# Performance work log

Measured on AMD Instinct MI355X. Metric: run time of the kernel, lower is better.

The kernel has to match this reference:

```python
import jax, jax.numpy as jnp
import numpy as np
from jax import lax

BN_EPS = 1e-5
NORM_EPS = 1e-8


def _conv(x, w, b, stride, pad):
    y = lax.conv_general_dilated(x, w, (stride, stride), [(pad, pad), (pad, pad)],
                                 dimension_numbers=('NCHW', 'OIHW', 'NCHW'))
    return y + b[None, :, None, None]


def _bn(x, g, b, m, v):
    inv = g / jnp.sqrt(v + BN_EPS)
    return x * inv[None, :, None, None] + (b - m * inv)[None, :, None, None]


def _maxpool2(x):
    return lax.reduce_window(x, -jnp.inf, lax.max, (1, 1, 2, 2), (1, 1, 2, 2), 'VALID')


def setup_inputs() -> dict:
    key = jax.random.key(0)
    ks = jax.random.split(key, 16)
    d = {}
    d['x'] = jax.random.normal(ks[0], (64, 3, 512, 512), dtype=jnp.float32)
    d['conv1_w'] = jax.random.normal(ks[1], (32, 1, 5, 5), jnp.float32) * 0.1
    d['conv1_b'] = jnp.zeros((32,), jnp.float32)
    d['bn1_g'] = jnp.ones((32,), jnp.float32)
    d['bn1_b'] = jnp.zeros((32,), jnp.float32)
    d['bn1_m'] = jax.random.normal(ks[2], (32,), jnp.float32) * 0.1
    d['bn1_v'] = jax.random.uniform(ks[3], (32,), jnp.float32) + 0.5
    d['conv2_w'] = jax.random.normal(ks[4], (64, 32, 3, 3), jnp.float32) * 0.05
    d['conv2_b'] = jnp.zeros((64,), jnp.float32)
    d['bn2_g'] = jnp.ones((64,), jnp.float32)
    d['bn2_b'] = jnp.zeros((64,), jnp.float32)
    d['bn2_m'] = jax.random.normal(ks[5], (64,), jnp.float32) * 0.1
    d['bn2_v'] = jax.random.uniform(ks[6], (64,), jnp.float32) + 0.5
    d['conv3_w'] = jax.random.normal(ks[7], (128, 64, 3, 3), jnp.float32) * 0.04
    d['conv3_b'] = jnp.zeros((128,), jnp.float32)
    d['bn3_g'] = jnp.ones((128,), jnp.float32)
    d['bn3_b'] = jnp.zeros((128,), jnp.float32)
    d['bn3_m'] = jax.random.normal(ks[8], (128,), jnp.float32) * 0.1
    d['bn3_v'] = jax.random.uniform(ks[9], (128,), jnp.float32) + 0.5
    d['fc1_w'] = jax.random.normal(ks[10], (256, 128), jnp.float32) * 0.08
    d['fc1_b'] = jnp.zeros((256,), jnp.float32)
    d['fc2_w'] = jax.random.normal(ks[11], (128, 256), jnp.float32) * 0.06
    d['fc2_b'] = jnp.zeros((128,), jnp.float32)
    return d


def reference(x, conv1_w, conv1_b, bn1_g, bn1_b, bn1_m, bn1_v,
              conv2_w, conv2_b, bn2_g, bn2_b, bn2_m, bn2_v,
              conv3_w, conv3_b, bn3_g, bn3_b, bn3_m, bn3_v,
              fc1_w, fc1_b, fc2_w, fc2_b):
    # ---- batched FFT feature extraction (replaces per-sample numpy loop) ----
    gray = 0.299 * x[:, 0] + 0.587 * x[:, 1] + 0.114 * x[:, 2]      # (B,H,W)
    mag = jnp.abs(jnp.fft.fftshift(jnp.fft.fft2(gray), axes=(-2, -1)))
    logm = jnp.log1p(mag)
    mu = logm.mean(axis=(-2, -1), keepdims=True)
    sd = logm.std(axis=(-2, -1), keepdims=True)
    f = ((logm - mu) / (sd + NORM_EPS))[:, None]                     # (B,1,H,W)
    # ---- conv stack (BatchNorm in inference mode) ----
    h = jax.nn.relu(_bn(_conv(f, conv1_w, conv1_b, 2, 2), bn1_g, bn1_b, bn1_m, bn1_v))
    h = _maxpool2(h)
    h = jax.nn.relu(_bn(_conv(h, conv2_w, conv2_b, 2, 1), bn2_g, bn2_b, bn2_m, bn2_v))
    h = _maxpool2(h)
    h = jax.nn.relu(_bn(_conv(h, conv3_w, conv3_b, 2, 1), bn3_g, bn3_b, bn3_m, bn3_v))
    h = h.mean(axis=(-2, -1))                                        # AdaptiveAvgPool2d(1) -> (B,128)
    # ---- MLP (Dropout is identity in eval) ----
    h = jax.nn.relu(h @ fc1_w.T + fc1_b)
    return jax.nn.relu(h @ fc2_w.T + fc2_b)
```

## Files before the change

kernel.cpp:

```cpp
#include <hip/hip_runtime.h>
#include <math.h>

#define PI_F 3.14159265358979323846f
#define KS 258

typedef float f2 __attribute__((ext_vector_type(2)));

__device__ __forceinline__ void fft512(float* re, float* im,
                                       const float* twr, const float* twi, int u) {
#pragma unroll
  for (int s = 0; s < 8; s += 2) {
    __syncthreads();
    {
      int h  = 1 << s;
      int j  = u & (h - 1);
      int a  = ((u >> s) << (s + 2)) + j;
      int i0 = a, i1 = a + h, i2 = a + 2 * h, i3 = a + 3 * h;
      float e0r = re[i0], e0i = im[i0];
      float e1r = re[i1], e1i = im[i1];
      float e2r = re[i2], e2i = im[i2];
      float e3r = re[i3], e3i = im[i3];
      int tis = j << (8 - s);
      float wsr = twr[tis], wsi = twi[tis];
      float t1r = e1r * wsr - e1i * wsi, t1i = e1r * wsi + e1i * wsr;
      float t3r = e3r * wsr - e3i * wsi, t3i = e3r * wsi + e3i * wsr;
      float b0r = e0r + t1r, b0i = e0i + t1i;
      float b1r = e0r - t1r, b1i = e0i - t1i;
      float b2r = e2r + t3r, b2i = e2i + t3i;
      float b3r = e2r - t3r, b3i = e2i - t3i;
      int ti0 = j << (7 - s);
      int ti1 = (j + h) << (7 - s);
      float w0r = twr[ti0], w0i = twi[ti0];
      float w1r = twr[ti1], w1i = twi[ti1];
      float u2r = b2r * w0r - b2i * w0i, u2i = b2r * w0i + b2i * w0r;
      float u3r = b3r * w1r - b3i * w1i, u3i = b3r * w1i + b3i * w1r;
      re[i0] = b0r + u2r; im[i0] = b0i + u2i;
      re[i2] = b0r - u2r; im[i2] = b0i - u2i;
      re[i1] = b1r + u3r; im[i1] = b1i + u3i;
      re[i3] = b1r - u3r; im[i3] = b1i - u3i;
    }
  }
  __syncthreads();
  {
#pragma unroll
    for (int k = 0; k < 2; ++k) {
      int i1 = u + k * 128;
      int i2 = i1 + 256;
      float wr = twr[i1], wi = twi[i1];
      float ur = re[i1], ui = im[i1];
      float vr = re[i2], vi = im[i2];
      float tr = vr * wr - vi * wi;
      float tq = vr * wi + vi * wr;
      re[i1] = ur + tr; im[i1] = ui + tq;
      re[i2] = ur - tr; im[i2] = ui - tq;
    }
  }
  __syncthreads();
}

__device__ __forceinline__ void init_tw(float* twr, float* twi, int t) {
  float s, c;
  sincosf(-2.0f * PI_F * (float)t * (1.0f / 512.0f), &s, &c);
  twr[t] = c; twi[t] = s;
}

__global__ __launch_bounds__(256) void k_rowfft(const float* __restrict__ x,
                                                float2* __restrict__ G) {
  __shared__ float re[1024], im[1024], twr[256], twi[256];
  int t = threadIdx.x;
  int q = blockIdx.x;
  int b = blockIdx.y;
  int f = t >> 7, u = t & 127;
  int r0 = 4 * q;
  const float* xb = x + ((size_t)b * 3 * 512 + r0) * 512;
  const float* xr = xb + (2 * f) * 512;
  float* reb = re + 512 * f;
  float* imb = im + 512 * f;
#pragma unroll
  for (int j = 0; j < 4; ++j) {
    int p = u + 128 * j;
    float a = 0.299f * xr[p]        + 0.587f * xr[262144 + p]  + 0.114f * xr[524288 + p];
    float c = 0.299f * xr[512 + p]  + 0.587f * xr[262656 + p]  + 0.114f * xr[524800 + p];
    int rv = __brev((unsigned)p) >> 23;
    reb[rv] = a; imb[rv] = c;
  }
  init_tw(twr, twi, t);
  fft512(reb, imb, twr, twi, u);
  int r0p = r0 + 2 * f;
  float2* G0 = G + ((size_t)b * 512 + r0p) * KS;
  float2* G1 = G0 + KS;
  for (int k = u; k <= 256; k += 128) {
    int mk = (512 - k) & 511;
    float zr = reb[k], zi = imb[k];
    float mr = reb[mk], mi = imb[mk];
    G0[k] = make_float2(0.5f * (zr + mr), 0.5f * (zi - mi));
    G1[k] = make_float2(0.5f * (zi + mi), 0.5f * (mr - zr));
  }
}

__global__ __launch_bounds__(256) void k_transpose(const float2* __restrict__ G,
                                                   float2* __restrict__ GT) {
  __shared__ float2 ta[32][33];
  int kt = blockIdx.x, rt = blockIdx.y, b = blockIdx.z;
  int tx = threadIdx.x, ty = threadIdx.y;
  int k0 = kt * 32, r0 = rt * 32;
  const float2* Gb = G + (size_t)b * 512 * KS;
  float2* GTb = GT + (size_t)b * KS * 512;
#pragma unroll
  for (int i = 0; i < 32; i += 8) {
    int k = k0 + tx;
    float2 v = make_float2(0.0f, 0.0f);
    if (k < KS) v = Gb[(size_t)(r0 + ty + i) * KS + k];
    ta[ty + i][tx] = v;
  }
  __syncthreads();
#pragma unroll
  for (int i = 0; i < 32; i += 8) {
    int k = k0 + ty + i;
    if (k < KS) GTb[(size_t)k * 512 + r0 + tx] = ta[tx][ty + i];
  }
}

__global__ __launch_bounds__(256) void k_colfft(const float2* __restrict__ GT,
                                                float* __restrict__ S,
                                                double* __restrict__ stats) {
  __shared__ float re[1024], im[1024], twr[256], twi[256];
  __shared__ float ws1[4], ws2[4];
  int t  = threadIdx.x;
  int b  = blockIdx.y;
  int f = t >> 7, u = t & 127;
  int kc = 2 * blockIdx.x + f;
  bool valid = (kc <= 256);
  const float2* Gc = GT + ((size_t)b * KS + kc) * 512;
  float* reb = re + 512 * f;
  float* imb = im + 512 * f;
#pragma unroll
  for (int j = 0; j < 4; ++j) {
    int p = u + 128 * j;
    float2 v = Gc[p];
    int rv = __brev((unsigned)p) >> 23;
    reb[rv] = v.x; imb[rv] = v.y;
  }
  init_tw(twr, twi, t);
  fft512(reb, imb, twr, twi, u);
  int vrow = (kc + 256) & 511;
  bool mir = (kc >= 1) && (kc <= 255);
  float* Sb = S + (size_t)b * 262144;
  float s1 = 0.0f, s2 = 0.0f;
#pragma unroll
  for (int j = 0; j < 4; ++j) {
    int k = u + 128 * j;
    float mm = log1pf(sqrtf(reb[k] * reb[k] + imb[k] * imb[k]));
    if (valid) {
      Sb[(size_t)vrow * 512 + ((k + 256) & 511)] = mm;
      if (mir) Sb[(size_t)(256 - kc) * 512 + ((256 - k) & 511)] = mm;
      s1 += mm; s2 += mm * mm;
    }
  }
  float w = mir ? 2.0f : (valid ? 1.0f : 0.0f);
  s1 *= w; s2 *= w;
#pragma unroll
  for (int off = 32; off > 0; off >>= 1) {
    s1 += __shfl_down(s1, off);
    s2 += __shfl_down(s2, off);
  }
  int wvid = t >> 6;
  if ((t & 63) == 0) { ws1[wvid] = s1; ws2[wvid] = s2; }
  __syncthreads();
  if (t == 0) {
    float a = ws1[0] + ws1[1] + ws1[2] + ws1[3];
    float c = ws2[0] + ws2[1] + ws2[2] + ws2[3];
    atomicAdd(&stats[2 * b],     (double)a);
    atomicAdd(&stats[2 * b + 1], (double)c);
  }
}

__global__ void k_zero_stats(double* stats) {
  stats[threadIdx.x] = 0.0;
}

__global__ void k_stats(const double* __restrict__ stats, float2* __restrict__ muinv) {
  int i = threadIdx.x;
  double n  = 262144.0;
  double mu = stats[2 * i] / n;
  double va = stats[2 * i + 1] / n - mu * mu;
  if (va < 0.0) va = 0.0;
  double sd = sqrt(va);
  muinv[i] = make_float2((float)mu, (float)(1.0 / (sd + 1e-8)));
}

#define TS1 68
__global__ __launch_bounds__(256) void k_conv1(
    const float* __restrict__ S, const float2* __restrict__ muinv,
    const float* __restrict__ w, const float* __restrict__ cb,
    const float* __restrict__ g, const float* __restrict__ bb,
    const float* __restrict__ bm, const float* __restrict__ bv,
    float* __restrict__ h1) {
  __shared__ float tile[67 * TS1];
  int b = blockIdx.y;
  int by = blockIdx.x >> 3, bx = blockIdx.x & 7;
  int y0 = by * 16, x0 = bx * 16;
  int h0 = 4 * y0 - 2, w0 = 4 * x0 - 2;
  float2 mi = muinv[b];
  const float* Sb = S + (size_t)b * 262144;
  for (int idx = threadIdx.x; idx < 67 * 67; idx += 256) {
    int wl = idx / 67, hl = idx - wl * 67;
    int hh = h0 + hl, ww = w0 + wl;
    float val = 0.0f;
    if (hh >= 0 && hh < 512 && ww >= 0 && ww < 512)
      val = (Sb[(size_t)ww * 512 + hh] - mi.x) * mi.y;
    tile[wl * TS1 + hl] = val;
  }
  __syncthreads();
  int ty = threadIdx.x >> 4, tx = threadIdx.x & 15;
  float in[7][7];
#pragma unroll
  for (int j = 0; j < 7; ++j)
#pragma unroll
    for (int i = 0; i < 7; ++i)
      in[i][j] = tile[(4 * tx + j) * TS1 + 4 * ty + i];
  f2 P[7][5];
#pragma unroll
  for (int r = 0; r < 7; ++r)
#pragma unroll
    for (int c = 0; c < 5; ++c)
      P[r][c] = (f2){in[r][c], in[r][c + 2]};
  int Y = y0 + ty, X = x0 + tx;
  for (int oc = 0; oc < 32; ++oc) {
    const float* wo = w + oc * 25;
    f2 aA = (f2){0.0f, 0.0f};
    f2 aB = (f2){0.0f, 0.0f};
#pragma unroll
    for (int dy = 0; dy < 5; ++dy)
#pragma unroll
      for (int dx = 0; dx < 5; ++dx) {
        float wv = wo[dy * 5 + dx];
        f2 wv2 = (f2){wv, wv};
        aA = __builtin_elementwise_fma(wv2, P[dy][dx],     aA);
        aB = __builtin_elementwise_fma(wv2, P[dy + 2][dx], aB);
      }
    float m   = fmaxf(fmaxf(aA.x, aA.y), fmaxf(aB.x, aB.y));
    float inv = g[oc] / sqrtf(bv[oc] + 1e-5f);
    float sh  = cb[oc] * inv + bb[oc] - bm[oc] * inv;
    h1[(((size_t)b * 32 + oc) * 128 + Y) * 128 + X] = fmaxf(m * inv + sh, 0.0f);
  }
}

#define TS2 36
__global__ __launch_bounds__(512) void k_conv2(
    const float* __restrict__ h1, const float* __restrict__ w,
    const float* __restrict__ cb, const float* __restrict__ g,
    const float* __restrict__ bb, const float* __restrict__ bm,
    const float* __restrict__ bv, float* __restrict__ h2) {
  __shared__ __attribute__((aligned(16))) float tile[8 * 33 * TS2];
  int tid = threadIdx.x;
  int b = blockIdx.y;
  int rt = blockIdx.x >> 2, ct = blockIdx.x & 3;
  int ty0 = rt * 16, tx0 = ct * 16;
  int wv = tid >> 6;
  int lane = tid & 63;
  int qy = lane >> 3, qx = lane & 7;
  int iy0 = 2 * ty0 - 1, ix0 = 2 * tx0 - 1;
  int ocbase = wv * 8;
  f2 accA[8], accB[8];
#pragma unroll
  for (int q = 0; q < 8; ++q) {
    accA[q] = (f2){0.0f, 0.0f};
    accB[q] = (f2){0.0f, 0.0f};
  }

  float rv[18];
  const size_t hb = (size_t)b * 32;

#define C2_LOADR(ICT)                                                          \
  {                                                                            \
    _Pragma("unroll")                                                          \
    for (int k = 0; k < 17; ++k) {                                             \
      int idx = tid + 512 * k;                                                 \
      int ic = idx / 1089;                                                     \
      int rem = idx - ic * 1089;                                               \
      int rr = rem / 33, cc = rem - rr * 33;                                   \
      int iy = iy0 + rr, ix = ix0 + cc;                                        \
      float v = 0.0f;                                                          \
      if (iy >= 0 && iy < 128 && ix >= 0 && ix < 128)                          \
        v = h1[((hb + (ICT) * 8 + ic) * 128 + iy) * 128 + ix];                 \
      rv[k] = v;                                                               \
    }                                                                          \
    if (tid < 8) {                                                             \
      int idx = 8704 + tid;                                                    \
      int ic = idx / 1089;                                                     \
      int rem = idx - ic * 1089;                                               \
      int rr = rem / 33, cc = rem - rr * 33;                                   \
      int iy = iy0 + rr, ix = ix0 + cc;                                        \
      float v = 0.0f;                                                          \
      if (iy >= 0 && iy < 128 && ix >= 0 && ix < 128)                          \
        v = h1[((hb + (ICT) * 8 + ic) * 128 + iy) * 128 + ix];                 \
      rv[17] = v;                                                              \
    }                                                                          \
  }

#define C2_WRITER()                                                            \
  {                                                                            \
    _Pragma("unroll")                                                          \
    for (int k = 0; k < 17; ++k) {                                             \
      int idx = tid + 512 * k;                                                 \
      int ic = idx / 1089;                                                     \
      int rem = idx - ic * 1089;                                               \
      int rr = rem / 33, cc = rem - rr * 33;                                   \
      tile[(ic * 33 + rr) * TS2 + cc] = rv[k];                                 \
    }                                                                          \
    if (tid < 8) {                                                             \
      int idx = 8704 + tid;                                                    \
      int ic = idx / 1089;                                                     \
      int rem = idx - ic * 1089;                                               \
      int rr = rem / 33, cc = rem - rr * 33;                                   \
      tile[(ic * 33 + rr) * TS2 + cc] = rv[17];                                \
    }                                                                          \
  }

  C2_LOADR(0);
  for (int ict = 0; ict < 4; ++ict) {
    __syncthreads();
    C2_WRITER();
    __syncthreads();
    if (ict < 3) C2_LOADR(ict + 1);
    int rbase = 4 * qy, cbase = 4 * qx;
#pragma unroll
    for (int ic = 0; ic < 8; ++ic) {
      int icg = ict * 8 + ic;
      f2 P[5][3];
#pragma unroll
      for (int i = 0; i < 5; ++i) {
        int base = (ic * 33 + rbase + i) * TS2 + cbase;
        float4 a = *reinterpret_cast<const float4*>(&tile[base]);
        float b4 = tile[base + 4];
        P[i][0] = (f2){a.x, a.z};
        P[i][1] = (f2){a.y, a.w};
        P[i][2] = (f2){a.z, b4};
      }
      const float* wic = w + ((size_t)ocbase * 32 + icg) * 9;
#pragma unroll
      for (int q = 0; q < 8; ++q) {
        const float* wo = wic + (size_t)q * 32 * 9;
#pragma unroll
        for (int dy = 0; dy < 3; ++dy)
#pragma unroll
          for (int dx = 0; dx < 3; ++dx) {
            float wvv = wo[dy * 3 + dx];
            f2 wv2 = (f2){wvv, wvv};
            accA[q] = __builtin_elementwise_fma(wv2, P[dy][dx],     accA[q]);
            accB[q] = __builtin_elementwise_fma(wv2, P[dy + 2][dx], accB[q]);
          }
      }
    }
  }
  int Yp = (ty0 >> 1) + qy, Xp = (tx0 >> 1) + qx;
#pragma unroll
  for (int q = 0; q < 8; ++q) {
    int oc = ocbase + q;
    float m   = fmaxf(fmaxf(accA[q].x, accA[q].y), fmaxf(accB[q].x, accB[q].y));
    float inv = g[oc] / sqrtf(bv[oc] + 1e-5f);
    float sh  = cb[oc] * inv + bb[oc] - bm[oc] * inv;
    h2[(((size_t)b * 64 + oc) * 32 + Yp) * 32 + Xp] = fmaxf(m * inv + sh, 0.0f);
  }
#undef C2_LOADR
#undef C2_WRITER
}

#define TS3 34
__global__ __launch_bounds__(256) void k_conv3(
    const float* __restrict__ h2, const float* __restrict__ w,
    const float* __restrict__ cb, const float* __restrict__ g,
    const float* __restrict__ bb, const float* __restrict__ bm,
    const float* __restrict__ bv, float* __restrict__ gap) {
  __shared__ __attribute__((aligned(16))) float tile[8 * 33 * TS3];
  __shared__ float ws3[8][4];
  int tid = threadIdx.x;
  int ocg = blockIdx.x, b = blockIdx.y;
  int cy = tid >> 4, cx = tid & 15;
  f2 accP[4];
#pragma unroll
  for (int qp = 0; qp < 4; ++qp) accP[qp] = (f2){0.0f, 0.0f};

  for (int ict = 0; ict < 8; ++ict) {
    __syncthreads();
    for (int idx = tid; idx < 8 * 33 * 33; idx += 256) {
      int ic = idx / 1089;
      int rem = idx - ic * 1089;
      int rr = rem / 33, cc = rem - rr * 33;
      int iy = rr - 1, ix = cc - 1;
      float v = 0.0f;
      int icg = ict * 8 + ic;
      if (iy >= 0 && iy < 32 && ix >= 0 && ix < 32)
        v = h2[(((size_t)b * 64 + icg) * 32 + iy) * 32 + ix];
      tile[(ic * 33 + rr) * TS3 + cc] = v;
    }
    __syncthreads();
#pragma unroll
    for (int ic = 0; ic < 8; ++ic) {
      int icg = ict * 8 + ic;
      float in[3][3];
#pragma unroll
      for (int i = 0; i < 3; ++i) {
        const float2* r2 = reinterpret_cast<const float2*>(&tile[(ic * 33 + 2 * cy + i) * TS3 + 2 * cx]);
        float2 a = r2[0];
        in[i][0] = a.x; in[i][1] = a.y;
        in[i][2] = tile[(ic * 33 + 2 * cy + i) * TS3 + 2 * cx + 2];
      }
      const float* wic = w + ((size_t)(ocg * 8) * 64 + icg) * 9;
#pragma unroll
      for (int qp = 0; qp < 4; ++qp) {
        const float* wo0 = wic + (size_t)(2 * qp) * 64 * 9;
        const float* wo1 = wo0 + 64 * 9;
#pragma unroll
        for (int i = 0; i < 3; ++i)
#pragma unroll
          for (int j = 0; j < 3; ++j) {
            f2 wp = (f2){wo0[i * 3 + j], wo1[i * 3 + j]};
            f2 iv = (f2){in[i][j], in[i][j]};
            accP[qp] = __builtin_elementwise_fma(wp, iv, accP[qp]);
          }
      }
    }
  }
  int wvid = tid >> 6;
#pragma unroll
  for (int q = 0; q < 8; ++q) {
    int oc = ocg * 8 + q;
    float a = (q & 1) ? accP[q >> 1].y : accP[q >> 1].x;
    float inv = g[oc] / sqrtf(bv[oc] + 1e-5f);
    float sh  = cb[oc] * inv + bb[oc] - bm[oc] * inv;
    float v = fmaxf(a * inv + sh, 0.0f);
#pragma unroll
    for (int off = 32; off > 0; off >>= 1) v += __shfl_down(v, off);
    if ((tid & 63) == 0) ws3[q][wvid] = v;
  }
  __syncthreads();
  if (tid < 8)
    gap[(size_t)b * 128 + ocg * 8 + tid] =
        (ws3[tid][0] + ws3[tid][1] + ws3[tid][2] + ws3[tid][3]) * (1.0f / 256.0f);
}

__global__ __launch_bounds__(256) void k_fc(
    const float* __restrict__ gap,
    const float* __restrict__ w1, const float* __restrict__ b1,
    const float* __restrict__ w2, const float* __restrict__ b2,
    float* __restrict__ out) {
  __shared__ float gv[128], hv[256];
  int b = blockIdx.x, t = threadIdx.x;
  if (t < 128) gv[t] = gap[(size_t)b * 128 + t];
  __syncthreads();
  float a1 = b1[t];
  const float* wr = w1 + (size_t)t * 128;
  for (int k = 0; k < 128; ++k) a1 = fmaf(wr[k], gv[k], a1);
  hv[t] = fmaxf(a1, 0.0f);
  __syncthreads();
  if (t < 128) {
    float a2 = b2[t];
    const float* wr2 = w2 + (size_t)t * 256;
    for (int k = 0; k < 256; ++k) a2 = fmaf(wr2[k], hv[k], a2);
    out[(size_t)b * 128 + t] = fmaxf(a2, 0.0f);
  }
}

extern "C" void kernel_launch(void* const* d_in, const int* in_sizes, int n_in,
                              void* d_out, int out_size, void* d_ws, size_t ws_size,
                              hipStream_t stream) {
  (void)in_sizes; (void)n_in; (void)out_size; (void)ws_size;
  const float* x   = (const float*)d_in[0];
  const float* c1w = (const float*)d_in[1];
  const float* c1b = (const float*)d_in[2];
  const float* b1g = (const float*)d_in[3];
  const float* b1b = (const float*)d_in[4];
  const float* b1m = (const float*)d_in[5];
  const float* b1v = (const float*)d_in[6];
  const float* c2w = (const float*)d_in[7];
  const float* c2b = (const float*)d_in[8];
  const float* b2g = (const float*)d_in[9];
  const float* b2b = (const float*)d_in[10];
  const float* b2m = (const float*)d_in[11];
  const float* b2v = (const float*)d_in[12];
  const float* c3w = (const float*)d_in[13];
  const float* c3b = (const float*)d_in[14];
  const float* b3g = (const float*)d_in[15];
  const float* b3b = (const float*)d_in[16];
  const float* b3m = (const float*)d_in[17];
  const float* b3v = (const float*)d_in[18];
  const float* f1w = (const float*)d_in[19];
  const float* f1b = (const float*)d_in[20];
  const float* f2w = (const float*)d_in[21];
  const float* f2b = (const float*)d_in[22];
  float* out = (float*)d_out;

  char* ws = (char*)d_ws;
  float2* G     = (float2*)(ws + 0);
  float2* GT    = (float2*)(ws + 67633152ull);
  float*  S     = (float*) (ws + 135266304ull);
  double* stats = (double*)(ws + 202375168ull);
  float2* muinv = (float2*)(ws + 202376192ull);
  float*  gap   = (float*) (ws + 202376704ull);
  float*  h1    = (float*) (ws + 0);
  float*  h2    = (float*) (ws + 135266304ull);

  k_zero_stats<<<1, 128, 0, stream>>>(stats);
  k_rowfft   <<<dim3(128, 64), 256, 0, stream>>>(x, G);
  k_transpose<<<dim3(9, 16, 64), dim3(32, 8), 0, stream>>>(G, GT);
  k_colfft   <<<dim3(129, 64), 256, 0, stream>>>(GT, S, stats);
  k_stats    <<<1, 64, 0, stream>>>(stats, muinv);
  k_conv1    <<<dim3(64, 64), 256, 0, stream>>>(S, muinv, c1w, c1b, b1g, b1b, b1m, b1v, h1);
  k_conv2    <<<dim3(16, 64), 512, 0, stream>>>(h1, c2w, c2b, b2g, b2b, b2m, b2v, h2);
  k_conv3    <<<dim3(16, 64), 256, 0, stream>>>(h2, c3w, c3b, b3g, b3b, b3m, b3v, gap);
  k_fc       <<<64, 256, 0, stream>>>(gap, f1w, f1b, f2w, f2b, out);
}
```

Before: 887.5 us.

## Double-buffer conv2 shared tile and precompute load/store offsets

Conv2 now keeps two shared-memory tile buffers, so each iteration writes the next input-channel chunk into the alternate buffer and needs only one barrier per iteration instead of two. The global-source and LDS-destination offsets are computed once into per-thread arrays rather than redone with integer divisions on every load and write. This doubles LDS use (about 76 KB per block) and adds 36 registers of offsets, which may lower occupancy.

Result: no change. 902.4 us (+1.7%).

```diff
diff --git a/kernel.cpp b/kernel.cpp
--- a/kernel.cpp
+++ b/kernel.cpp
@@ -252,7 +252,7 @@
     const float* __restrict__ cb, const float* __restrict__ g,
     const float* __restrict__ bb, const float* __restrict__ bm,
     const float* __restrict__ bv, float* __restrict__ h2) {
-  __shared__ __attribute__((aligned(16))) float tile[8 * 33 * TS2];
+  __shared__ __attribute__((aligned(16))) float tile[2][8 * 33 * TS2];
   int tid = threadIdx.x;
   int b = blockIdx.y;
   int rt = blockIdx.x >> 2, ct = blockIdx.x & 3;
@@ -269,76 +269,69 @@
     accB[q] = (f2){0.0f, 0.0f};
   }
 
+  int dsto[18], srco[18];
+#pragma unroll
+  for (int k = 0; k < 17; ++k) {
+    int idx = tid + 512 * k;
+    int ic = idx / 1089;
+    int rem = idx - ic * 1089;
+    int rr = rem / 33, cc = rem - rr * 33;
+    int iy = iy0 + rr, ix = ix0 + cc;
+    dsto[k] = (ic * 33 + rr) * TS2 + cc;
+    srco[k] = (iy >= 0 && iy < 128 && ix >= 0 && ix < 128)
+                  ? ((ic * 128 + iy) * 128 + ix) : -1;
+  }
+  {
+    int idx = 8704 + tid;
+    int ic = idx / 1089;
+    int rem = idx - ic * 1089;
+    int rr = rem / 33, cc = rem - rr * 33;
+    int iy = iy0 + rr, ix = ix0 + cc;
+    dsto[17] = (ic * 33 + rr) * TS2 + cc;
+    srco[17] = (tid < 8 && iy >= 0 && iy < 128 && ix >= 0 && ix < 128)
+                   ? ((ic * 128 + iy) * 128 + ix) : -1;
+  }
+  const float* h1b = h1 + (size_t)b * 32 * 16384;
+
   float rv[18];
-  const size_t hb = (size_t)b * 32;
-
 #define C2_LOADR(ICT)                                                          \
   {                                                                            \
     _Pragma("unroll")                                                          \
-    for (int k = 0; k < 17; ++k) {                                             \
-      int idx = tid + 512 * k;                                                 \
-      int ic = idx / 1089;                                                     \
-      int rem = idx - ic * 1089;                                               \
-      int rr = rem / 33, cc = rem - rr * 33;                                   \
-      int iy = iy0 + rr, ix = ix0 + cc;                                        \
+    for (int k = 0; k < 18; ++k) {                                             \
       float v = 0.0f;                                                          \
-      if (iy >= 0 && iy < 128 && ix >= 0 && ix < 128)                          \
-        v = h1[((hb + (ICT) * 8 + ic) * 128 + iy) * 128 + ix];                 \
+      if (srco[k] >= 0) v = h1b[(ICT) * 131072 + srco[k]];                     \
       rv[k] = v;                                                               \
     }                                                                          \
-    if (tid < 8) {                                                             \
-      int idx = 8704 + tid;                                                    \
-      int ic = idx / 1089;                                                     \
-      int rem = idx - ic * 1089;                                               \
-      int rr = rem / 33, cc = rem - rr * 33;                                   \
-      int iy = iy0 + rr, ix = ix0 + cc;                                        \
-      float v = 0.0f;                                                          \
-      if (iy >= 0 && iy < 128 && ix >= 0 && ix < 128)                          \
-        v = h1[((hb + (ICT) * 8 + ic) * 128 + iy) * 128 + ix];                 \
-      rv[17] = v;                                                              \
-    }                                                                          \
-  }
-
-#define C2_WRITER()                                                            \
+  }
+
+#define C2_WRITER(BUF)                                                         \
   {                                                                            \
     _Pragma("unroll")                                                          \
-    for (int k = 0; k < 17; ++k) {                                             \
-      int idx = tid + 512 * k;                                                 \
-      int ic = idx / 1089;                                                     \
-      int rem = idx - ic * 1089;                                               \
-      int rr = rem / 33, cc = rem - rr * 33;                                   \
-      tile[(ic * 33 + rr) * TS2 + cc] = rv[k];                                 \
-    }                                                                          \
-    if (tid < 8) {                                                             \
-      int idx = 8704 + tid;                                                    \
-      int ic = idx / 1089;                                                     \
-      int rem = idx - ic * 1089;                                               \
-      int rr = rem / 33, cc = rem - rr * 33;                                   \
-      tile[(ic * 33 + rr) * TS2 + cc] = rv[17];                                \
-    }                                                                          \
+    for (int k = 0; k < 17; ++k) tile[BUF][dsto[k]] = rv[k];                   \
+    if (tid < 8) tile[BUF][dsto[17]] = rv[17];                                 \
   }
 
   C2_LOADR(0);
   for (int ict = 0; ict < 4; ++ict) {
+    int bs = ict & 1;
+    C2_WRITER(bs);
+    if (ict < 3) C2_LOADR(ict + 1);
     __syncthreads();
-    C2_WRITER();
-    __syncthreads();
-    if (ict < 3) C2_LOADR(ict + 1);
+    const float* tb = tile[bs];
     int rbase = 4 * qy, cbase = 4 * qx;
 #pragma unroll
     for (int ic = 0; ic < 8; ++ic) {
-      int icg = ict * 8 + ic;
       f2 P[5][3];
 #pragma unroll
       for (int i = 0; i < 5; ++i) {
         int base = (ic * 33 + rbase + i) * TS2 + cbase;
-        float4 a = *reinterpret_cast<const float4*>(&tile[base]);
-        float b4 = tile[base + 4];
+        float4 a = *reinterpret_cast<const float4*>(&tb[base]);
+        float b4 = tb[base + 4];
         P[i][0] = (f2){a.x, a.z};
         P[i][1] = (f2){a.y, a.w};
         P[i][2] = (f2){a.z, b4};
       }
-      const float* wic = w + ((size_t)ocbase * 32 + icg) * 9;
+      const float* wic = w + ((size_t)ocbase * 32 + ict * 8 + ic) * 9;
 #pragma unroll
       for (int q = 0; q < 8; ++q) {
         const float* wo = wic + (size_t)q * 32 * 9;
```
